# Performance work log

Measured on AMD Instinct MI355X. Metric: run time of the kernel, lower is better.

Reference implementation:

```python
import jax, jax.numpy as jnp
import numpy as np

E = 256      # feat_dim
H = 4        # num_heads
D = E // H   # head_dim = 64
NC = 7       # num_classes
B = 65536
EPS = 1e-5


def layernorm(x, g, b):
    mu = jnp.mean(x, axis=-1, keepdims=True)
    var = jnp.mean((x - mu) ** 2, axis=-1, keepdims=True)
    return (x - mu) * jax.lax.rsqrt(var + EPS) * g + b


def setup_inputs() -> dict:
    key = jax.random.key(0)
    ks = jax.random.split(key, 16)
    s = 0.02
    return {
        "f_swin":   jax.random.normal(ks[0], (B, E), jnp.float32),
        "f_maxvit": jax.random.normal(ks[1], (B, E), jnp.float32),
        "f_focal":  jax.random.normal(ks[2], (B, E), jnp.float32),
        # MultiheadAttention params (torch packs q,k,v into in_proj)
        "in_proj_w": jax.random.normal(ks[3], (3 * E, E), jnp.float32) * s,
        "in_proj_b": jnp.zeros((3 * E,), jnp.float32),
        "out_w": jax.random.normal(ks[4], (E, E), jnp.float32) * s,
        "out_b": jnp.zeros((E,), jnp.float32),
        # fusion LayerNorm
        "ln1_g": jnp.ones((E,), jnp.float32),
        "ln1_b": jnp.zeros((E,), jnp.float32),
        # gate: Linear(3E, 3)
        "gate_w": jax.random.normal(ks[5], (3, 3 * E), jnp.float32) * s,
        "gate_b": jnp.zeros((3,), jnp.float32),
        # deep_head: LN -> Linear(E,256) -> GELU -> Linear(256,128) -> GELU -> Linear(128,7)
        "ln2_g": jnp.ones((E,), jnp.float32),
        "ln2_b": jnp.zeros((E,), jnp.float32),
        "w1": jax.random.normal(ks[6], (256, E), jnp.float32) * s,
        "b1": jnp.zeros((256,), jnp.float32),
        "w2": jax.random.normal(ks[7], (128, 256), jnp.float32) * s,
        "b2": jnp.zeros((128,), jnp.float32),
        "w3": jax.random.normal(ks[8], (NC, 128), jnp.float32) * s,
        "b3": jnp.zeros((NC,), jnp.float32),
    }


def reference(f_swin, f_maxvit, f_focal, in_proj_w, in_proj_b, out_w, out_b,
              ln1_g, ln1_b, gate_w, gate_b, ln2_g, ln2_b,
              w1, b1, w2, b2, w3, b3):
    # --- AttentionFusionModule ---
    stacked = jnp.stack([f_swin, f_maxvit, f_focal], axis=1)  # [B,3,E]
    qkv = stacked @ in_proj_w.T + in_proj_b                   # [B,3,3E]
    q, k, v = jnp.split(qkv, 3, axis=-1)
    # [B,3,E] -> [B,H,3,D]
    def to_heads(t):
        return t.reshape(t.shape[0], 3, H, D).transpose(0, 2, 1, 3)
    qh, kh, vh = to_heads(q), to_heads(k), to_heads(v)
    scores = jnp.einsum('bhqd,bhkd->bhqk', qh, kh) / jnp.sqrt(jnp.float32(D))
    attn = jax.nn.softmax(scores, axis=-1)
    ctx = jnp.einsum('bhqk,bhkd->bhqd', attn, vh)             # [B,H,3,D]
    ctx = ctx.transpose(0, 2, 1, 3).reshape(-1, 3, E)         # [B,3,E]
    att_out = ctx @ out_w.T + out_b
    x = layernorm(att_out + stacked, ln1_g, ln1_b)            # [B,3,E]
    concat = jnp.concatenate([f_swin, f_maxvit, f_focal], axis=-1)  # [B,3E]
    weights = jax.nn.softmax(concat @ gate_w.T + gate_b, axis=-1)   # [B,3]
    fused = jnp.einsum('bse,bs->be', x, weights)              # [B,E]
    # --- deep_head (Dropout inactive at inference; exact GELU as in torch) ---
    h = layernorm(fused, ln2_g, ln2_b)
    h = jax.nn.gelu(h @ w1.T + b1, approximate=False)
    h = jax.nn.gelu(h @ w2.T + b2, approximate=False)
    logits = h @ w3.T + b3
    return logits, fused
```

## Files before the change

### kernel.cpp

```cpp
#include <hip/hip_runtime.h>
#include <math.h>


#define E   256
#define NC  7
#define BM  16
#define TOK 48
#define NT  256
#define BS  264

typedef unsigned short u16;
typedef unsigned int   u32;
typedef __attribute__((ext_vector_type(8))) short  short8;
typedef __attribute__((ext_vector_type(4))) float  f32x4;

#define O_IPW 0
#define O_OW  196608
#define O_GW  262144
#define O_W1  264448
#define O_W2  329984
#define CVT_TOTAL 362752

__device__ __forceinline__ float bf2f(u32 u) { return __uint_as_float(u << 16); }
__device__ __forceinline__ u16 f2bf(float f) {
    u32 u = __float_as_uint(f);
    return (u16)((u + 0x7fffu + ((u >> 16) & 1u)) >> 16);
}

__global__ void cvt_weights(const float* __restrict__ ipw, const float* __restrict__ ow,
                            const float* __restrict__ gw,  const float* __restrict__ w1,
                            const float* __restrict__ w2,  u16* __restrict__ ws) {
    int i4 = (blockIdx.x * 256 + threadIdx.x) * 4;
    if (i4 >= CVT_TOTAL) return;
    const float* src; int off;
    if      (i4 < O_OW)  { src = ipw; off = i4; }
    else if (i4 < O_GW)  { src = ow;  off = i4 - O_OW; }
    else if (i4 < O_W1)  { src = gw;  off = i4 - O_GW; }
    else if (i4 < O_W2)  { src = w1;  off = i4 - O_W1; }
    else                 { src = w2;  off = i4 - O_W2; }
    float4 v = *(const float4*)(src + off);
    ushort4 o;
    o.x = f2bf(v.x); o.y = f2bf(v.y); o.z = f2bf(v.z); o.w = f2bf(v.w);
    *(ushort4*)(ws + i4) = o;
}

template<int NTW>
__device__ __forceinline__ void issue_b(const u16* __restrict__ bW, int rowBase, int lane,
                                        short8 (&b)[8][NTW]) {
    const int l16 = lane & 15, quad = lane >> 4;
    #pragma unroll
    for (int ks = 0; ks < 8; ++ks)
        #pragma unroll
        for (int j = 0; j < NTW; ++j)
            b[ks][j] = *(const short8*)(bW + (size_t)(rowBase + j * 16 + l16) * 256 + ks * 32 + quad * 8);
}

template<int MT, int NTW>
__device__ __forceinline__ void consume_gemm(const u16* aLds, int aRow0, int lane,
                                             const short8 (&b)[8][NTW], f32x4 (&acc)[MT][NTW]) {
    const int l16 = lane & 15, quad = lane >> 4;
    #pragma unroll
    for (int m = 0; m < MT; ++m)
        #pragma unroll
        for (int j = 0; j < NTW; ++j) acc[m][j] = (f32x4){0.f, 0.f, 0.f, 0.f};
    #pragma unroll
    for (int ks = 0; ks < 8; ++ks) {
        short8 a[MT];
        #pragma unroll
        for (int m = 0; m < MT; ++m)
            a[m] = *(const short8*)(aLds + (size_t)(aRow0 + m * 16 + l16) * BS + ks * 32 + quad * 8);
        #pragma unroll
        for (int j = 0; j < NTW; ++j)
            #pragma unroll
            for (int m = 0; m < MT; ++m)
                acc[m][j] = __builtin_amdgcn_mfma_f32_16x16x32_bf16(a[m], b[ks][j], acc[m][j], 0, 0, 0);
    }
}

__global__ __launch_bounds__(NT, 2)
void dhc_mfma_kernel(
    const float* __restrict__ f0, const float* __restrict__ f1, const float* __restrict__ f2,
    const float* __restrict__ ipb, const float* __restrict__ ob,
    const float* __restrict__ ln1g, const float* __restrict__ ln1b,
    const float* __restrict__ gb,
    const float* __restrict__ ln2g, const float* __restrict__ ln2b,
    const float* __restrict__ b1, const float* __restrict__ b2,
    const float* __restrict__ w3, const float* __restrict__ b3,
    const u16* __restrict__ ws, float* __restrict__ d_out, int nrows)
{
    __shared__ __align__(16) u16 s_x[TOK * BS];
    __shared__ __align__(16) u16 s_buf[TOK * BS];
    __shared__ float s_attn[BM][4][9];
    __shared__ float s_gp[BM][9];
    __shared__ float s_wgt[BM][3];
    __shared__ float s_mu[TOK], s_rstd[TOK];
    __shared__ float s_mu2[BM], s_rstd2[BM];

    const int tid  = threadIdx.x;
    const int wid  = tid >> 6, lane = tid & 63;
    const int l16  = lane & 15, quad = lane >> 4;
    const long long row0 = (long long)blockIdx.x * BM;
    const size_t fused_base = (size_t)nrows * NC;

    const u16* ipw_b = ws + O_IPW;
    const u16* ow_b  = ws + O_OW;
    const u16* gw_b  = ws + O_GW;
    const u16* w1_b  = ws + O_W1;
    const u16* w2_b  = ws + O_W2;

    short8 bq[8][4];
    short8 b5[8][2];

    const int rb0 = (wid < 2) ? (64 * wid) : (256 + 64 * (wid - 2));

    issue_b<4>(ipw_b, rb0, lane, bq);

    #pragma unroll
    for (int it = 0; it < 12; ++it) {
        int id = it * NT + tid;
        int t  = id >> 6;
        int c4 = (id & 63) * 4;
        int s  = t >> 4, r = t & 15;
        float4 v = {0.f, 0.f, 0.f, 0.f};
        if (row0 + r < nrows) {
            const float* src = (s == 0 ? f0 : (s == 1 ? f1 : f2));
            v = *(const float4*)(src + (size_t)(row0 + r) * E + c4);
        }
        ushort4 o;
        o.x = f2bf(v.x); o.y = f2bf(v.y); o.z = f2bf(v.z); o.w = f2bf(v.w);
        *(ushort4*)(s_x + t * BS + c4) = o;
    }
    __syncthreads();

    for (int p = 0; p < 2; ++p) {
        const int rb = rb0 + 128 * p;
        f32x4 acc[3][4];
        consume_gemm<3, 4>(s_x, 0, lane, bq, acc);
        issue_b<4>(ipw_b, (p == 0) ? (rb0 + 128) : (512 + 64 * wid), lane, bq);
        #pragma unroll
        for (int j = 0; j < 4; ++j) {
            int n = wid * 64 + j * 16 + l16;
            float bias = ipb[rb + j * 16 + l16];
            #pragma unroll
            for (int m = 0; m < 3; ++m)
                #pragma unroll
                for (int rr = 0; rr < 4; ++rr) {
                    int tok = m * 16 + quad * 4 + rr;
                    s_buf[tok * BS + n] = f2bf(acc[m][j][rr] + bias);
                }
        }
        __syncthreads();
        if (tid < 96) {
            int r = tid / 6, rem = tid % 6;
            int hh = rem / 3, i = rem % 3;
            int h = 2 * p + hh;
            float d0 = 0.f, d1 = 0.f, d2 = 0.f;
            const u16* qrow = s_buf + (i * 16 + r) * BS + hh * 64;
            const u16* k0 = s_buf + (0 * 16 + r) * BS + 128 + hh * 64;
            const u16* k1 = s_buf + (1 * 16 + r) * BS + 128 + hh * 64;
            const u16* k2 = s_buf + (2 * 16 + r) * BS + 128 + hh * 64;
            for (int d8 = 0; d8 < 8; ++d8) {
                short8 qv = *(const short8*)(qrow + d8 * 8);
                short8 a0 = *(const short8*)(k0 + d8 * 8);
                short8 a1 = *(const short8*)(k1 + d8 * 8);
                short8 a2 = *(const short8*)(k2 + d8 * 8);
                #pragma unroll
                for (int e = 0; e < 8; ++e) {
                    float q = bf2f((u32)(u16)qv[e]);
                    d0 += q * bf2f((u32)(u16)a0[e]);
                    d1 += q * bf2f((u32)(u16)a1[e]);
                    d2 += q * bf2f((u32)(u16)a2[e]);
                }
            }
            d0 *= 0.125f; d1 *= 0.125f; d2 *= 0.125f;
            float mx = fmaxf(d0, fmaxf(d1, d2));
            float e0 = expf(d0 - mx), e1 = expf(d1 - mx), e2 = expf(d2 - mx);
            float inv = 1.f / (e0 + e1 + e2);
            s_attn[r][h][i * 3 + 0] = e0 * inv;
            s_attn[r][h][i * 3 + 1] = e1 * inv;
            s_attn[r][h][i * 3 + 2] = e2 * inv;
        }
        __syncthreads();
    }

    {
        const int rb = 512 + 64 * wid;
        f32x4 acc[3][4];
        consume_gemm<3, 4>(s_x, 0, lane, bq, acc);
        issue_b<4>(ow_b, 64 * wid, lane, bq);
        #pragma unroll
        for (int j = 0; j < 4; ++j) {
            int n = wid * 64 + j * 16 + l16;
            float bias = ipb[rb + j * 16 + l16];
            #pragma unroll
            for (int m = 0; m < 3; ++m)
                #pragma unroll
                for (int rr = 0; rr < 4; ++rr) {
                    int tok = m * 16 + quad * 4 + rr;
                    s_buf[tok * BS + n] = f2bf(acc[m][j][rr] + bias);
                }
        }
    }
    __syncthreads();

    {
        int r = tid >> 4;
        int cb = (tid & 15) * 16;
        int h = cb >> 6;
        float a[9];
        #pragma unroll
        for (int q2 = 0; q2 < 9; ++q2) a[q2] = s_attn[r][h][q2];
        #pragma unroll
        for (int cc = 0; cc < 16; ++cc) {
            int c = cb + cc;
            float v0 = bf2f((u32)s_buf[(0 * 16 + r) * BS + c]);
            float v1 = bf2f((u32)s_buf[(1 * 16 + r) * BS + c]);
            float v2 = bf2f((u32)s_buf[(2 * 16 + r) * BS + c]);
            float c0 = a[0] * v0 + a[1] * v1 + a[2] * v2;
            float c1 = a[3] * v0 + a[4] * v1 + a[5] * v2;
            float c2 = a[6] * v0 + a[7] * v1 + a[8] * v2;
            s_buf[(0 * 16 + r) * BS + c] = f2bf(c0);
            s_buf[(1 * 16 + r) * BS + c] = f2bf(c1);
            s_buf[(2 * 16 + r) * BS + c] = f2bf(c2);
        }
    }
    __syncthreads();

    {
        const int rb = 64 * wid;
        f32x4 acc[3][4];
        consume_gemm<3, 4>(s_buf, 0, lane, bq, acc);
        issue_b<4>(w1_b, 64 * wid, lane, bq);
        #pragma unroll
        for (int j = 0; j < 4; ++j) {
            int n = rb + j * 16 + l16;
            float bias = ob[n];
            #pragma unroll
            for (int m = 0; m < 3; ++m)
                #pragma unroll
                for (int rr = 0; rr < 4; ++rr) {
                    int tok = m * 16 + quad * 4 + rr;
                    acc[m][j][rr] += bias + bf2f((u32)s_x[tok * BS + n]);
                }
        }
        __syncthreads();
        #pragma unroll
        for (int j = 0; j < 4; ++j) {
            int n = rb + j * 16 + l16;
            #pragma unroll
            for (int m = 0; m < 3; ++m)
                #pragma unroll
                for (int rr = 0; rr < 4; ++rr) {
                    int tok = m * 16 + quad * 4 + rr;
                    s_buf[tok * BS + n] = f2bf(acc[m][j][rr]);
                }
        }
    }
    __syncthreads();

    if (tid < TOK) {
        const u16* xp = s_buf + tid * BS;
        float sum = 0.f, sq = 0.f;
        for (int c8 = 0; c8 < 32; ++c8) {
            short8 v = *(const short8*)(xp + c8 * 8);
            #pragma unroll
            for (int e = 0; e < 8; ++e) {
                float x = bf2f((u32)(u16)v[e]);
                sum += x; sq += x * x;
            }
        }
        float mu = sum * (1.f / 256.f);
        float var = sq * (1.f / 256.f) - mu * mu;
        s_mu[tid] = mu;
        s_rstd[tid] = rsqrtf(var + 1e-5f);
    }
    __syncthreads();
    {
        float g = ln1g[tid], b = ln1b[tid];
        #pragma unroll 4
        for (int t = 0; t < TOK; ++t) {
            float x = bf2f((u32)s_buf[t * BS + tid]);
            s_buf[t * BS + tid] = f2bf((x - s_mu[t]) * s_rstd[t] * g + b);
        }
    }
    __syncthreads();

    if (tid < 144) {
        int r = tid / 9, rem = tid % 9;
        int g = rem / 3, s = rem % 3;
        const u16* xp = s_x + (s * 16 + r) * BS;
        const u16* wp = gw_b + g * 768 + s * 256;
        float acc = 0.f;
        for (int c8 = 0; c8 < 32; ++c8) {
            short8 xv = *(const short8*)(xp + c8 * 8);
            short8 wv = *(const short8*)(wp + c8 * 8);
            #pragma unroll
            for (int e = 0; e < 8; ++e)
                acc += bf2f((u32)(u16)xv[e]) * bf2f((u32)(u16)wv[e]);
        }
        s_gp[r][g * 3 + s] = acc;
    }
    __syncthreads();
    if (tid < 48) {
        int r = tid / 3, g = tid % 3;
        s_wgt[r][g] = gb[g] + s_gp[r][g * 3 + 0] + s_gp[r][g * 3 + 1] + s_gp[r][g * 3 + 2];
    }
    __syncthreads();
    if (tid < BM) {
        float l0 = s_wgt[tid][0], l1 = s_wgt[tid][1], l2 = s_wgt[tid][2];
        float mx = fmaxf(l0, fmaxf(l1, l2));
        float e0 = expf(l0 - mx), e1 = expf(l1 - mx), e2 = expf(l2 - mx);
        float inv = 1.f / (e0 + e1 + e2);
        s_wgt[tid][0] = e0 * inv; s_wgt[tid][1] = e1 * inv; s_wgt[tid][2] = e2 * inv;
    }
    __syncthreads();

    {
        int c = tid;
        float* outF = d_out + fused_base;
        #pragma unroll 4
        for (int r = 0; r < BM; ++r) {
            float f = s_wgt[r][0] * bf2f((u32)s_buf[(0 * 16 + r) * BS + c])
                    + s_wgt[r][1] * bf2f((u32)s_buf[(1 * 16 + r) * BS + c])
                    + s_wgt[r][2] * bf2f((u32)s_buf[(2 * 16 + r) * BS + c]);
            if (row0 + r < nrows) outF[(size_t)(row0 + r) * E + c] = f;
            s_buf[r * BS + c] = f2bf(f);
        }
    }
    __syncthreads();

    if (tid < BM) {
        const u16* fp = s_buf + tid * BS;
        float sum = 0.f, sq = 0.f;
        for (int c8 = 0; c8 < 32; ++c8) {
            short8 v = *(const short8*)(fp + c8 * 8);
            #pragma unroll
            for (int e = 0; e < 8; ++e) {
                float x = bf2f((u32)(u16)v[e]);
                sum += x; sq += x * x;
            }
        }
        float mu = sum * (1.f / 256.f);
        float var = sq * (1.f / 256.f) - mu * mu;
        s_mu2[tid] = mu;
        s_rstd2[tid] = rsqrtf(var + 1e-5f);
    }
    __syncthreads();
    {
        float g = ln2g[tid], b = ln2b[tid];
        #pragma unroll
        for (int r = 0; r < BM; ++r) {
            float x = bf2f((u32)s_buf[r * BS + tid]);
            s_buf[r * BS + tid] = f2bf((x - s_mu2[r]) * s_rstd2[r] * g + b);
        }
    }
    __syncthreads();

    {
        const int rb = 64 * wid;
        f32x4 acc[1][4];
        consume_gemm<1, 4>(s_buf, 0, lane, bq, acc);
        issue_b<2>(w2_b, 32 * wid, lane, b5);
        __syncthreads();
        #pragma unroll
        for (int j = 0; j < 4; ++j) {
            int n = rb + j * 16 + l16;
            float bias = b1[n];
            #pragma unroll
            for (int rr = 0; rr < 4; ++rr) {
                int r = quad * 4 + rr;
                float x = acc[0][j][rr] + bias;
                float hgelu = 0.5f * x * (1.f + erff(x * 0.70710678118654752f));
                s_buf[(16 + r) * BS + n] = f2bf(hgelu);
            }
        }
    }
    __syncthreads();

    {
        const int rb = 32 * wid;
        f32x4 acc[1][2];
        consume_gemm<1, 2>(s_buf, 16, lane, b5, acc);
        __syncthreads();
        #pragma unroll
        for (int j = 0; j < 2; ++j) {
            int n = rb + j * 16 + l16;
            float bias = b2[n];
            #pragma unroll
            for (int rr = 0; rr < 4; ++rr) {
                int r = quad * 4 + rr;
                float x = acc[0][j][rr] + bias;
                float hgelu = 0.5f * x * (1.f + erff(x * 0.70710678118654752f));
                s_buf[(32 + r) * BS + n] = f2bf(hgelu);
            }
        }
    }
    __syncthreads();

    if (tid < BM * NC) {
        int r = tid / NC, n = tid % NC;
        float acc = b3[n];
        const float* wr = w3 + n * 128;
        const u16* hp = s_buf + (32 + r) * BS;
        for (int k4 = 0; k4 < 32; ++k4) {
            float4 w = *(const float4*)(wr + k4 * 4);
            acc += bf2f((u32)hp[k4 * 4 + 0]) * w.x
                 + bf2f((u32)hp[k4 * 4 + 1]) * w.y
                 + bf2f((u32)hp[k4 * 4 + 2]) * w.z
                 + bf2f((u32)hp[k4 * 4 + 3]) * w.w;
        }
        if (row0 + r < nrows) d_out[(size_t)(row0 + r) * NC + n] = acc;
    }
}

extern "C" void kernel_launch(void* const* d_in, const int* in_sizes, int n_in,
                              void* d_out, int out_size, void* d_ws, size_t ws_size,
                              hipStream_t stream) {
    (void)n_in; (void)ws_size; (void)out_size;
    const int nrows = in_sizes[0] / E;
    u16* ws = (u16*)d_ws;
    cvt_weights<<<(CVT_TOTAL / 4 + 255) / 256, 256, 0, stream>>>(
        (const float*)d_in[3], (const float*)d_in[5], (const float*)d_in[9],
        (const float*)d_in[13], (const float*)d_in[15], ws);
    const int nblocks = (nrows + BM - 1) / BM;
    dhc_mfma_kernel<<<nblocks, NT, 0, stream>>>(
        (const float*)d_in[0], (const float*)d_in[1], (const float*)d_in[2],
        (const float*)d_in[4], (const float*)d_in[6],
        (const float*)d_in[7], (const float*)d_in[8],
        (const float*)d_in[10],
        (const float*)d_in[11], (const float*)d_in[12],
        (const float*)d_in[14], (const float*)d_in[16],
        (const float*)d_in[17], (const float*)d_in[18],
        ws, (float*)d_out, nrows);
}
```

Before: 720.1 us.

## Overlap gate logits with attention, parallelize LayerNorm stats, split accumulators

```diff
diff --git a/kernel.cpp b/kernel.cpp
--- a/kernel.cpp
+++ b/kernel.cpp
@@ -90,11 +90,12 @@
 {
     __shared__ __align__(16) u16 s_x[TOK * BS];
     __shared__ __align__(16) u16 s_buf[TOK * BS];
-    __shared__ float s_attn[BM][4][9];
-    __shared__ float s_gp[BM][9];
-    __shared__ float s_wgt[BM][3];
-    __shared__ float s_mu[TOK], s_rstd[TOK];
-    __shared__ float s_mu2[BM], s_rstd2[BM];
+    __shared__ __align__(16) float s_small[576];
+    #define S_ATTN(r,h,q) s_small[((r) * 4 + (h)) * 9 + (q)]
+    float* s_mu    = s_small;
+    float* s_rstd  = s_small + 48;
+    float* s_mu2   = s_small + 96;
+    float* s_rstd2 = s_small + 112;
 
     const int tid  = threadIdx.x;
     const int wid  = tid >> 6, lane = tid & 63;
@@ -102,6 +103,10 @@
     const long long row0 = (long long)blockIdx.x * BM;
     const size_t fused_base = (size_t)nrows * NC;
 
+    auto pad_slot = [&](int i) -> float* {
+        return (float*)(s_buf + (i >> 2) * BS + 256) + (i & 3);
+    };
+
     const u16* ipw_b = ws + O_IPW;
     const u16* ow_b  = ws + O_OW;
     const u16* gw_b  = ws + O_GW;
@@ -112,7 +117,6 @@
     short8 b5[8][2];
 
     const int rb0 = (wid < 2) ? (64 * wid) : (256 + 64 * (wid - 2));
-
     issue_b<4>(ipw_b, rb0, lane, bq);
 
     #pragma unroll
@@ -154,7 +158,7 @@
             int r = tid / 6, rem = tid % 6;
             int hh = rem / 3, i = rem % 3;
             int h = 2 * p + hh;
-            float d0 = 0.f, d1 = 0.f, d2 = 0.f;
+            float d0a = 0.f, d0b = 0.f, d1a = 0.f, d1b = 0.f, d2a = 0.f, d2b = 0.f;
             const u16* qrow = s_buf + (i * 16 + r) * BS + hh * 64;
             const u16* k0 = s_buf + (0 * 16 + r) * BS + 128 + hh * 64;
             const u16* k1 = s_buf + (1 * 16 + r) * BS + 128 + hh * 64;
@@ -165,20 +169,58 @@
                 short8 a1 = *(const short8*)(k1 + d8 * 8);
                 short8 a2 = *(const short8*)(k2 + d8 * 8);
                 #pragma unroll
-                for (int e = 0; e < 8; ++e) {
-                    float q = bf2f((u32)(u16)qv[e]);
-                    d0 += q * bf2f((u32)(u16)a0[e]);
-                    d1 += q * bf2f((u32)(u16)a1[e]);
-                    d2 += q * bf2f((u32)(u16)a2[e]);
-                }
-            }
-            d0 *= 0.125f; d1 *= 0.125f; d2 *= 0.125f;
+                for (int e = 0; e < 4; ++e) {
+                    float qa = bf2f((u32)(u16)qv[e]);
+                    float qb = bf2f((u32)(u16)qv[e + 4]);
+                    d0a += qa * bf2f((u32)(u16)a0[e]); d0b += qb * bf2f((u32)(u16)a0[e + 4]);
+                    d1a += qa * bf2f((u32)(u16)a1[e]); d1b += qb * bf2f((u32)(u16)a1[e + 4]);
+                    d2a += qa * bf2f((u32)(u16)a2[e]); d2b += qb * bf2f((u32)(u16)a2[e + 4]);
+                }
+            }
+            float d0 = (d0a + d0b) * 0.125f, d1 = (d1a + d1b) * 0.125f, d2 = (d2a + d2b) * 0.125f;
             float mx = fmaxf(d0, fmaxf(d1, d2));
-            float e0 = expf(d0 - mx), e1 = expf(d1 - mx), e2 = expf(d2 - mx);
+            float e0 = __expf(d0 - mx), e1 = __expf(d1 - mx), e2 = __expf(d2 - mx);
             float inv = 1.f / (e0 + e1 + e2);
-            s_attn[r][h][i * 3 + 0] = e0 * inv;
-            s_attn[r][h][i * 3 + 1] = e1 * inv;
-            s_attn[r][h][i * 3 + 2] = e2 * inv;
+            S_ATTN(r, h, i * 3 + 0) = e0 * inv;
+            S_ATTN(r, h, i * 3 + 1) = e1 * inv;
+            S_ATTN(r, h, i * 3 + 2) = e2 * inv;
+        } else if (p == 0 && tid < 240) {
+            int idx = tid - 96;
+            int r = idx / 9, rem = idx % 9;
+            int g = rem / 3, s = rem % 3;
+            const u16* xp = s_x + (s * 16 + r) * BS;
+            const u16* wp = gw_b + g * 768 + s * 256;
+            float a0 = 0.f, a1 = 0.f, a2 = 0.f, a3 = 0.f;
+            for (int c8 = 0; c8 < 8; ++c8) {
+                #pragma unroll
+                for (int q4 = 0; q4 < 4; ++q4) {
+                    short8 xv = *(const short8*)(xp + (c8 * 4 + q4) * 8);
+                    short8 wv = *(const short8*)(wp + (c8 * 4 + q4) * 8);
+                    float t = 0.f;
+                    #pragma unroll
+                    for (int e = 0; e < 8; ++e)
+                        t += bf2f((u32)(u16)xv[e]) * bf2f((u32)(u16)wv[e]);
+                    if      (q4 == 0) a0 += t;
+                    else if (q4 == 1) a1 += t;
+                    else if (q4 == 2) a2 += t;
+                    else              a3 += t;
+                }
+            }
+            *pad_slot(idx) = (a0 + a1) + (a2 + a3);
+        } else if (p == 1 && tid < 112) {
+            int r = tid - 96;
+            float l[3];
+            #pragma unroll
+            for (int g = 0; g < 3; ++g)
+                l[g] = gb[g] + *pad_slot(r * 9 + g * 3 + 0)
+                             + *pad_slot(r * 9 + g * 3 + 1)
+                             + *pad_slot(r * 9 + g * 3 + 2);
+            float mx = fmaxf(l[0], fmaxf(l[1], l[2]));
+            float e0 = __expf(l[0] - mx), e1 = __expf(l[1] - mx), e2 = __expf(l[2] - mx);
+            float inv = 1.f / (e0 + e1 + e2);
+            *pad_slot(144 + r * 3 + 0) = e0 * inv;
+            *pad_slot(144 + r * 3 + 1) = e1 * inv;
+            *pad_slot(144 + r * 3 + 2) = e2 * inv;
         }
         __syncthreads();
     }
@@ -209,7 +251,7 @@
         int h = cb >> 6;
         float a[9];
         #pragma unroll
-        for (int q2 = 0; q2 < 9; ++q2) a[q2] = s_attn[r][h][q2];
+        for (int q2 = 0; q2 < 9; ++q2) a[q2] = S_ATTN(r, h, q2);
         #pragma unroll
         for (int cc = 0; cc < 16; ++cc) {
             int c = cb + cc;
@@ -258,21 +300,30 @@
     }
     __syncthreads();
 
-    if (tid < TOK) {
-        const u16* xp = s_buf + tid * BS;
-        float sum = 0.f, sq = 0.f;
-        for (int c8 = 0; c8 < 32; ++c8) {
+    if (tid < 192) {
+        int r = tid >> 2, j = tid & 3;
+        const u16* xp = s_buf + r * BS + j * 64;
+        float s0 = 0.f, s1 = 0.f, q0 = 0.f, q1 = 0.f;
+        #pragma unroll
+        for (int c8 = 0; c8 < 8; ++c8) {
             short8 v = *(const short8*)(xp + c8 * 8);
             #pragma unroll
-            for (int e = 0; e < 8; ++e) {
-                float x = bf2f((u32)(u16)v[e]);
-                sum += x; sq += x * x;
-            }
-        }
-        float mu = sum * (1.f / 256.f);
-        float var = sq * (1.f / 256.f) - mu * mu;
-        s_mu[tid] = mu;
-        s_rstd[tid] = rsqrtf(var + 1e-5f);
+            for (int e = 0; e < 4; ++e) {
+                float xa = bf2f((u32)(u16)v[e]);
+                float xb = bf2f((u32)(u16)v[e + 4]);
+                s0 += xa; q0 += xa * xa;
+                s1 += xb; q1 += xb * xb;
+            }
+        }
+        float sum = s0 + s1, sq = q0 + q1;
+        sum += __shfl_xor(sum, 1); sq += __shfl_xor(sq, 1);
+        sum += __shfl_xor(sum, 2); sq += __shfl_xor(sq, 2);
+        if (j == 0) {
+            float mu = sum * (1.f / 256.f);
+            float var = sq * (1.f / 256.f) - mu * mu;
+            s_mu[r] = mu;
+            s_rstd[r] = rsqrtf(var + 1e-5f);
+        }
     }
     __syncthreads();
     {
@@ -285,54 +336,29 @@
     }
     __syncthreads();
 
-    if (tid < 144) {
-        int r = tid / 9, rem = tid % 9;
-        int g = rem / 3, s = rem % 3;
-        const u16* xp = s_x + (s * 16 + r) * BS;
-        const u16* wp = gw_b + g * 768 + s * 256;
-        float acc = 0.f;
-        for (int c8 = 0; c8 < 32; ++c8) {
-            short8 xv = *(const short8*)(xp + c8 * 8);
-            short8 wv = *(const short8*)(wp + c8 * 8);
-            #pragma unroll
-            for (int e = 0; e < 8; ++e)
-                acc += bf2f((u32)(u16)xv[e]) * bf2f((u32)(u16)wv[e]);
-        }
-        s_gp[r][g * 3 + s] = acc;
-    }
-    __syncthreads();
-    if (tid < 48) {
-        int r = tid / 3, g = tid % 3;
-        s_wgt[r][g] = gb[g] + s_gp[r][g * 3 + 0] + s_gp[r][g * 3 + 1] + s_gp[r][g * 3 + 2];
-    }
-    __syncthreads();
-    if (tid < BM) {
-        float l0 = s_wgt[tid][0], l1 = s_wgt[tid][1], l2 = s_wgt[tid][2];
-        float mx = fmaxf(l0, fmaxf(l1, l2));
-        float e0 = expf(l0 - mx), e1 = expf(l1 - mx), e2 = expf(l2 - mx);
-        float inv = 1.f / (e0 + e1 + e2);
-        s_wgt[tid][0] = e0 * inv; s_wgt[tid][1] = e1 * inv; s_wgt[tid][2] = e2 * inv;
-    }
-    __syncthreads();
-
     {
         int c = tid;
         float* outF = d_out + fused_base;
         #pragma unroll 4
         for (int r = 0; r < BM; ++r) {
-            float f = s_wgt[r][0] * bf2f((u32)s_buf[(0 * 16 + r) * BS + c])
-                    + s_wgt[r][1] * bf2f((u32)s_buf[(1 * 16 + r) * BS + c])
-                    + s_wgt[r][2] * bf2f((u32)s_buf[(2 * 16 + r) * BS + c]);
+            float w0 = *pad_slot(144 + r * 3 + 0);
+            float w1v = *pad_slot(144 + r * 3 + 1);
+            float w2v = *pad_slot(144 + r * 3 + 2);
+            float f = w0  * bf2f((u32)s_buf[(0 * 16 + r) * BS + c])
+                    + w1v * bf2f((u32)s_buf[(1 * 16 + r) * BS + c])
+                    + w2v * bf2f((u32)s_buf[(2 * 16 + r) * BS + c]);
             if (row0 + r < nrows) outF[(size_t)(row0 + r) * E + c] = f;
             s_buf[r * BS + c] = f2bf(f);
         }
     }
     __syncthreads();
 
-    if (tid < BM) {
-        const u16* fp = s_buf + tid * BS;
+    {
+        int r = tid >> 4, j = tid & 15;
+        const u16* fp = s_buf + r * BS + j * 16;
         float sum = 0.f, sq = 0.f;
-        for (int c8 = 0; c8 < 32; ++c8) {
+        #pragma unroll
+        for (int c8 = 0; c8 < 2; ++c8) {
             short8 v = *(const short8*)(fp + c8 * 8);
             #pragma unroll
             for (int e = 0; e < 8; ++e) {
@@ -340,10 +366,16 @@
                 sum += x; sq += x * x;
             }
         }
-        float mu = sum * (1.f / 256.f);
-        float var = sq * (1.f / 256.f) - mu * mu;
-        s_mu2[tid] = mu;
-        s_rstd2[tid] = rsqrtf(var + 1e-5f);
+        sum += __shfl_xor(sum, 1); sq += __shfl_xor(sq, 1);
+        sum += __shfl_xor(sum, 2); sq += __shfl_xor(sq, 2);
+        sum += __shfl_xor(sum, 4); sq += __shfl_xor(sq, 4);
+        sum += __shfl_xor(sum, 8); sq += __shfl_xor(sq, 8);
+        if (j == 0) {
+            float mu = sum * (1.f / 256.f);
+            float var = sq * (1.f / 256.f) - mu * mu;
+            s_mu2[r] = mu;
+            s_rstd2[r] = rsqrtf(var + 1e-5f);
+        }
     }
     __syncthreads();
     {
@@ -399,16 +431,26 @@
 
     if (tid < BM * NC) {
         int r = tid / NC, n = tid % NC;
-        float acc = b3[n];
         const float* wr = w3 + n * 128;
         const u16* hp = s_buf + (32 + r) * BS;
-        for (int k4 = 0; k4 < 32; ++k4) {
-            float4 w = *(const float4*)(wr + k4 * 4);
-            acc += bf2f((u32)hp[k4 * 4 + 0]) * w.x
-                 + bf2f((u32)hp[k4 * 4 + 1]) * w.y
-                 + bf2f((u32)hp[k4 * 4 + 2]) * w.z
-                 + bf2f((u32)hp[k4 * 4 + 3]) * w.w;
-        }
+        float a0 = 0.f, a1 = 0.f, a2 = 0.f, a3 = 0.f;
+        #pragma unroll
+        for (int q8 = 0; q8 < 8; ++q8) {
+            #pragma unroll
+            for (int q4 = 0; q4 < 4; ++q4) {
+                int k4 = q8 * 4 + q4;
+                float4 w = *(const float4*)(wr + k4 * 4);
+                float t = bf2f((u32)hp[k4 * 4 + 0]) * w.x
+                        + bf2f((u32)hp[k4 * 4 + 1]) * w.y
+                        + bf2f((u32)hp[k4 * 4 + 2]) * w.z
+                        + bf2f((u32)hp[k4 * 4 + 3]) * w.w;
+                if      (q4 == 0) a0 += t;
+                else if (q4 == 1) a1 += t;
+                else if (q4 == 2) a2 += t;
+                else              a3 += t;
+            }
+        }
+        float acc = b3[n] + (a0 + a1) + (a2 + a3);
         if (row0 + r < nrows) d_out[(size_t)(row0 + r) * NC + n] = acc;
     }
 }
```

New measurement: 722.6 us. About the same (+0.4%).
